# Kernel tuning notes

Hardware: AMD Instinct MI355X
Metric: run time of the kernel (lower is better)

## Reference

```python
import jax, jax.numpy as jnp
import numpy as np

ALPHA = 0.1
STEPS = 4


def setup_inputs() -> dict:
    key = jax.random.key(0)
    x = jax.random.normal(key, (4, 8192, 1024), dtype=jnp.float32)
    return {"x": x}


def reference(x) -> jnp.ndarray:
    # CtaPostAttnMixer.forward, layout='bld', prefill, steps=4, alpha=0.1
    # Fixed-boundary 1D heat-diffusion stencil along the sequence dim.
    if x.shape[1] < 3:
        return x
    y = x.astype(jnp.float32)
    for _ in range(STEPS):
        # Laplacian on interior tokens: y[l+1] - 2 y[l] + y[l-1]
        lap = y[:, 2:, :] - 2.0 * y[:, 1:-1, :] + y[:, :-2, :]
        y = jnp.concatenate(
            [y[:, :1, :], y[:, 1:-1, :] + ALPHA * lap, y[:, -1:, :]], axis=1
        )
    return y.astype(x.dtype)
```

## Files before the change

kernel.cpp:

```cpp
#include <hip/hip_runtime.h>


namespace {

constexpr int Lr   = 8192;
constexpr int Dq   = 1024 / 4;
constexpr int Bn   = 4;
constexpr int C    = 4;
constexpr int W    = C + 8;
constexpr int SEGS = Lr / C;
constexpr int NXCD = 8;
constexpr int NWG  = SEGS * Bn;

constexpr float WK0 = 0.4870f;
constexpr float WK1 = 0.2144f;
constexpr float WK2 = 0.0388f;
constexpr float WK3 = 0.0032f;
constexpr float WK4 = 0.0001f;

__device__ __forceinline__ float4 f4_add(float4 a, float4 b) {
    return make_float4(a.x + b.x, a.y + b.y, a.z + b.z, a.w + b.w);
}
__device__ __forceinline__ float4 f4_mul(float s, float4 a) {
    return make_float4(s * a.x, s * a.y, s * a.z, s * a.w);
}
__device__ __forceinline__ float4 f4_fma(float s, float4 a, float4 c) {
    return make_float4(fmaf(s, a.x, c.x), fmaf(s, a.y, c.y),
                       fmaf(s, a.z, c.z), fmaf(s, a.w, c.w));
}

__global__ __launch_bounds__(256, 8)
void mixer4_kernel(const float4* __restrict__ x, float4* __restrict__ y) {
    const int d4  = threadIdx.x;

    const int lin = blockIdx.x;
    const int g   = (lin & (NXCD - 1)) * (NWG / NXCD) + (lin >> 3);
    const int b   = g >> 11;
    const int seg = g & (SEGS - 1);
    const int c0  = seg * C;

    const float4* __restrict__ xb = x + (size_t)b * Lr * Dq + d4;
    float4* __restrict__       yb = y + (size_t)b * Lr * Dq + d4;

    float4 w[W];
#pragma unroll
    for (int i = 0; i < W; ++i) {
        int gl = c0 - 4 + i;
        gl = gl < 0 ? 0 : gl;
        gl = gl > Lr - 1 ? Lr - 1 : gl;
        w[i] = xb[(size_t)gl * Dq];
    }
#pragma unroll
    for (int i = 0; i < W; ++i) {
        asm volatile("" : "+v"(w[i].x), "+v"(w[i].y), "+v"(w[i].z), "+v"(w[i].w));
    }

    if (c0 != 0 && c0 != Lr - C) {
#pragma unroll
        for (int j = 0; j < C; ++j) {
            float4 acc = f4_mul(WK0, w[j + 4]);
            acc = f4_fma(WK1, f4_add(w[j + 3], w[j + 5]), acc);
            acc = f4_fma(WK2, f4_add(w[j + 2], w[j + 6]), acc);
            acc = f4_fma(WK3, f4_add(w[j + 1], w[j + 7]), acc);
            acc = f4_fma(WK4, f4_add(w[j + 0], w[j + 8]), acc);
            yb[(size_t)(c0 + j) * Dq] = acc;
        }
    } else if (c0 == 0) {
        yb[0] = w[4];
        {
            float4 o = f4_mul(0.2986f, w[4]);
            o = f4_fma(0.4482f, w[5], o);
            o = f4_fma(0.2112f, w[6], o);
            o = f4_fma(0.0387f, w[7], o);
            o = f4_fma(0.0032f, w[8], o);
            o = f4_fma(0.0001f, w[9], o);
            yb[(size_t)1 * Dq] = o;
        }
        {
            float4 o = f4_mul(0.0454f, w[4]);
            o = f4_fma(0.2112f, w[5], o);
            o = f4_fma(0.4869f, w[6], o);
            o = f4_fma(0.2144f, w[7], o);
            o = f4_fma(0.0388f, w[8], o);
            o = f4_fma(0.0032f, w[9], o);
            o = f4_fma(0.0001f, w[10], o);
            yb[(size_t)2 * Dq] = o;
        }
        {
            float4 o = f4_mul(0.0034f, w[4]);
            o = f4_fma(0.0387f, w[5], o);
            o = f4_fma(0.2144f, w[6], o);
            o = f4_fma(0.4870f, w[7], o);
            o = f4_fma(0.2144f, w[8], o);
            o = f4_fma(0.0388f, w[9], o);
            o = f4_fma(0.0032f, w[10], o);
            o = f4_fma(0.0001f, w[11], o);
            yb[(size_t)3 * Dq] = o;
        }
    } else {
        yb[(size_t)(Lr - 1) * Dq] = w[7];
        {
            float4 o = f4_mul(0.2986f, w[7]);
            o = f4_fma(0.4482f, w[6], o);
            o = f4_fma(0.2112f, w[5], o);
            o = f4_fma(0.0387f, w[4], o);
            o = f4_fma(0.0032f, w[3], o);
            o = f4_fma(0.0001f, w[2], o);
            yb[(size_t)(Lr - 2) * Dq] = o;
        }
        {
            float4 o = f4_mul(0.0454f, w[7]);
            o = f4_fma(0.2112f, w[6], o);
            o = f4_fma(0.4869f, w[5], o);
            o = f4_fma(0.2144f, w[4], o);
            o = f4_fma(0.0388f, w[3], o);
            o = f4_fma(0.0032f, w[2], o);
            o = f4_fma(0.0001f, w[1], o);
            yb[(size_t)(Lr - 3) * Dq] = o;
        }
        {
            float4 o = f4_mul(0.0034f, w[7]);
            o = f4_fma(0.0387f, w[6], o);
            o = f4_fma(0.2144f, w[5], o);
            o = f4_fma(0.4870f, w[4], o);
            o = f4_fma(0.2144f, w[3], o);
            o = f4_fma(0.0388f, w[2], o);
            o = f4_fma(0.0032f, w[1], o);
            o = f4_fma(0.0001f, w[0], o);
            yb[(size_t)(Lr - 4) * Dq] = o;
        }
    }
}

}

extern "C" void kernel_launch(void* const* d_in, const int* in_sizes, int n_in,
                              void* d_out, int out_size, void* d_ws, size_t ws_size,
                              hipStream_t stream) {
    const float4* x = (const float4*)d_in[0];
    float4*       y = (float4*)d_out;

    dim3 grid(NWG);
    dim3 block(256);
    hipLaunchKernelGGL(mixer4_kernel, grid, block, 0, stream, x, y);
}
```

Measured before the change: 237.3 us.

## Stage 2D row-by-column tiles in LDS via direct global-to-LDS loads

Each block now handles a tile of 32 sequence rows by 64 float4 columns. It loads the 40-row haloed window into shared memory with global_load_lds, and each wavefront then computes 8 output rows from a 16-row register window. Before, every block read a 12-row window to write only 4 rows. The larger tiles cut halo re-reads from 3x to 1.25x of the input and reduce the block count. The cost is an LDS round trip, a barrier, and lower declared occupancy.

```diff
diff --git a/kernel.cpp b/kernel.cpp
--- a/kernel.cpp
+++ b/kernel.cpp
@@ -6,11 +6,13 @@
 constexpr int Lr   = 8192;
 constexpr int Dq   = 1024 / 4;
 constexpr int Bn   = 4;
-constexpr int C    = 4;
-constexpr int W    = C + 8;
-constexpr int SEGS = Lr / C;
+constexpr int R    = 32;
+constexpr int WR   = R + 8;
+constexpr int CW   = 64;
+constexpr int RT   = Lr / R;
+constexpr int CT   = Dq / CW;
 constexpr int NXCD = 8;
-constexpr int NWG  = SEGS * Bn;
+constexpr int NWG  = RT * CT * Bn;
 
 constexpr float WK0 = 0.4870f;
 constexpr float WK1 = 0.2144f;
@@ -29,106 +31,127 @@
                        fmaf(s, a.z, c.z), fmaf(s, a.w, c.w));
 }
 
-__global__ __launch_bounds__(256, 8)
+__global__ __launch_bounds__(256, 4)
 void mixer4_kernel(const float4* __restrict__ x, float4* __restrict__ y) {
-    const int d4  = threadIdx.x;
+    __shared__ float4 tile[WR][CW];
 
     const int lin = blockIdx.x;
     const int g   = (lin & (NXCD - 1)) * (NWG / NXCD) + (lin >> 3);
-    const int b   = g >> 11;
-    const int seg = g & (SEGS - 1);
-    const int c0  = seg * C;
+    const int rt  = g & (RT - 1);
+    const int bc  = g >> 8;
+    const int ct  = bc & (CT - 1);
+    const int b   = bc >> 2;
+    const int r0  = rt * R;
 
-    const float4* __restrict__ xb = x + (size_t)b * Lr * Dq + d4;
-    float4* __restrict__       yb = y + (size_t)b * Lr * Dq + d4;
+    const size_t origin = (size_t)b * Lr * Dq + (size_t)ct * CW;
+    const float4* __restrict__ xt = x + origin;
+    float4* __restrict__       yt = y + origin;
 
-    float4 w[W];
+    const int lane = threadIdx.x & 63;
+    const int wid  = threadIdx.x >> 6;
+
 #pragma unroll
-    for (int i = 0; i < W; ++i) {
-        int gl = c0 - 4 + i;
-        gl = gl < 0 ? 0 : gl;
-        gl = gl > Lr - 1 ? Lr - 1 : gl;
-        w[i] = xb[(size_t)gl * Dq];
+    for (int ii = 0; ii < WR / 4; ++ii) {
+        const int i  = wid + ii * 4;
+        int grow = r0 - 4 + i;
+        grow = grow < 0 ? 0 : grow;
+        grow = grow > Lr - 1 ? Lr - 1 : grow;
+        const float4* src = xt + (size_t)grow * Dq + lane;
+        __builtin_amdgcn_global_load_lds(
+            (const __attribute__((address_space(1))) void*)src,
+            (__attribute__((address_space(3))) void*)&tile[i][0],
+            16, 0, 0);
     }
+    __syncthreads();
+
+    const int kbase = wid * 8;
+    float4 win[16];
 #pragma unroll
-    for (int i = 0; i < W; ++i) {
-        asm volatile("" : "+v"(w[i].x), "+v"(w[i].y), "+v"(w[i].z), "+v"(w[i].w));
-    }
+    for (int i = 0; i < 16; ++i) win[i] = tile[kbase + i][lane];
 
-    if (c0 != 0 && c0 != Lr - C) {
-#pragma unroll
-        for (int j = 0; j < C; ++j) {
-            float4 acc = f4_mul(WK0, w[j + 4]);
-            acc = f4_fma(WK1, f4_add(w[j + 3], w[j + 5]), acc);
-            acc = f4_fma(WK2, f4_add(w[j + 2], w[j + 6]), acc);
-            acc = f4_fma(WK3, f4_add(w[j + 1], w[j + 7]), acc);
-            acc = f4_fma(WK4, f4_add(w[j + 0], w[j + 8]), acc);
-            yb[(size_t)(c0 + j) * Dq] = acc;
-        }
-    } else if (c0 == 0) {
-        yb[0] = w[4];
+    auto interior = [&](int j) {
+        float4 acc = f4_mul(WK0, win[j + 4]);
+        acc = f4_fma(WK1, f4_add(win[j + 3], win[j + 5]), acc);
+        acc = f4_fma(WK2, f4_add(win[j + 2], win[j + 6]), acc);
+        acc = f4_fma(WK3, f4_add(win[j + 1], win[j + 7]), acc);
+        acc = f4_fma(WK4, f4_add(win[j + 0], win[j + 8]), acc);
+        yt[(size_t)(r0 + kbase + j) * Dq + lane] = acc;
+    };
+
+    const bool low  = (r0 == 0)       && (wid == 0);
+    const bool high = (r0 == Lr - R)  && (wid == 3);
+
+    if (low) {
+        yt[0 * (size_t)Dq + lane] = win[4];
         {
-            float4 o = f4_mul(0.2986f, w[4]);
-            o = f4_fma(0.4482f, w[5], o);
-            o = f4_fma(0.2112f, w[6], o);
-            o = f4_fma(0.0387f, w[7], o);
-            o = f4_fma(0.0032f, w[8], o);
-            o = f4_fma(0.0001f, w[9], o);
-            yb[(size_t)1 * Dq] = o;
+            float4 o = f4_mul(0.2986f, win[4]);
+            o = f4_fma(0.4482f, win[5], o);
+            o = f4_fma(0.2112f, win[6], o);
+            o = f4_fma(0.0387f, win[7], o);
+            o = f4_fma(0.0032f, win[8], o);
+            o = f4_fma(0.0001f, win[9], o);
+            yt[1 * (size_t)Dq + lane] = o;
         }
         {
-            float4 o = f4_mul(0.0454f, w[4]);
-            o = f4_fma(0.2112f, w[5], o);
-            o = f4_fma(0.4869f, w[6], o);
-            o = f4_fma(0.2144f, w[7], o);
-            o = f4_fma(0.0388f, w[8], o);
-            o = f4_fma(0.0032f, w[9], o);
-            o = f4_fma(0.0001f, w[10], o);
-            yb[(size_t)2 * Dq] = o;
+            float4 o = f4_mul(0.0454f, win[4]);
+            o = f4_fma(0.2112f, win[5], o);
+            o = f4_fma(0.4869f, win[6], o);
+            o = f4_fma(0.2144f, win[7], o);
+            o = f4_fma(0.0388f, win[8], o);
+            o = f4_fma(0.0032f, win[9], o);
+            o = f4_fma(0.0001f, win[10], o);
+            yt[2 * (size_t)Dq + lane] = o;
         }
         {
-            float4 o = f4_mul(0.0034f, w[4]);
-            o = f4_fma(0.0387f, w[5], o);
-            o = f4_fma(0.2144f, w[6], o);
-            o = f4_fma(0.4870f, w[7], o);
-            o = f4_fma(0.2144f, w[8], o);
-            o = f4_fma(0.0388f, w[9], o);
-            o = f4_fma(0.0032f, w[10], o);
-            o = f4_fma(0.0001f, w[11], o);
-            yb[(size_t)3 * Dq] = o;
+            float4 o = f4_mul(0.0034f, win[4]);
+            o = f4_fma(0.0387f, win[5], o);
+            o = f4_fma(0.2144f, win[6], o);
+            o = f4_fma(0.4870f, win[7], o);
+            o = f4_fma(0.2144f, win[8], o);
+            o = f4_fma(0.0388f, win[9], o);
+            o = f4_fma(0.0032f, win[10], o);
+            o = f4_fma(0.0001f, win[11], o);
+            yt[3 * (size_t)Dq + lane] = o;
+        }
+#pragma unroll
+        for (int j = 4; j < 8; ++j) interior(j);
+    } else if (high) {
+#pragma unroll
+        for (int j = 0; j < 4; ++j) interior(j);
+        yt[(size_t)(Lr - 1) * Dq + lane] = win[11];
+        {
+            float4 o = f4_mul(0.2986f, win[11]);
+            o = f4_fma(0.4482f, win[10], o);
+            o = f4_fma(0.2112f, win[9], o);
+            o = f4_fma(0.0387f, win[8], o);
+            o = f4_fma(0.0032f, win[7], o);
+            o = f4_fma(0.0001f, win[6], o);
+            yt[(size_t)(Lr - 2) * Dq + lane] = o;
+        }
+        {
+            float4 o = f4_mul(0.0454f, win[11]);
+            o = f4_fma(0.2112f, win[10], o);
+            o = f4_fma(0.4869f, win[9], o);
+            o = f4_fma(0.2144f, win[8], o);
+            o = f4_fma(0.0388f, win[7], o);
+            o = f4_fma(0.0032f, win[6], o);
+            o = f4_fma(0.0001f, win[5], o);
+            yt[(size_t)(Lr - 3) * Dq + lane] = o;
+        }
+        {
+            float4 o = f4_mul(0.0034f, win[11]);
+            o = f4_fma(0.0387f, win[10], o);
+            o = f4_fma(0.2144f, win[9], o);
+            o = f4_fma(0.4870f, win[8], o);
+            o = f4_fma(0.2144f, win[7], o);
+            o = f4_fma(0.0388f, win[6], o);
+            o = f4_fma(0.0032f, win[5], o);
+            o = f4_fma(0.0001f, win[4], o);
+            yt[(size_t)(Lr - 4) * Dq + lane] = o;
         }
     } else {
-        yb[(size_t)(Lr - 1) * Dq] = w[7];
-        {
-            float4 o = f4_mul(0.2986f, w[7]);
-            o = f4_fma(0.4482f, w[6], o);
-            o = f4_fma(0.2112f, w[5], o);
-            o = f4_fma(0.0387f, w[4], o);
-            o = f4_fma(0.0032f, w[3], o);
-            o = f4_fma(0.0001f, w[2], o);
-            yb[(size_t)(Lr - 2) * Dq] = o;
-        }
-        {
-            float4 o = f4_mul(0.0454f, w[7]);
-            o = f4_fma(0.2112f, w[6], o);
-            o = f4_fma(0.4869f, w[5], o);
-            o = f4_fma(0.2144f, w[4], o);
-            o = f4_fma(0.0388f, w[3], o);
-            o = f4_fma(0.0032f, w[2], o);
-            o = f4_fma(0.0001f, w[1], o);
-            yb[(size_t)(Lr - 3) * Dq] = o;
-        }
-        {
-            float4 o = f4_mul(0.0034f, w[7]);
-            o = f4_fma(0.0387f, w[6], o);
-            o = f4_fma(0.2144f, w[5], o);
-            o = f4_fma(0.4870f, w[4], o);
-            o = f4_fma(0.2144f, w[3], o);
-            o = f4_fma(0.0388f, w[2], o);
-            o = f4_fma(0.0032f, w[1], o);
-            o = f4_fma(0.0001f, w[0], o);
-            yb[(size_t)(Lr - 4) * Dq] = o;
-        }
+#pragma unroll
+        for (int j = 0; j < 8; ++j) interior(j);
     }
 }
 
```

New measurement: 228.1 us. -3.9%, faster.
